# Optimization experiments

Hardware: AMD Instinct MI355X
Metric: run time of the kernel (lower is better)

Reference implementation:

```python
import jax, jax.numpy as jnp
import numpy as np

V, D, C, H = 32, 128, 2048, 8
B, M = 8, 2048
HD = D // H


def rms_norm(x, scale):
    # Whole-tensor (per-batch) RMS over dims (1,2), as in the source (quirky but faithful).
    Bx, Mx, Dx = x.shape
    fr = jnp.sqrt(jnp.sum(x * x, axis=(1, 2))) * (Mx * Dx) ** -0.5  # (B,)
    raw = x / fr[:, None, None]
    return scale[:Mx, :][None, :, :] * raw


def rope_tables(Mx):
    i = jnp.arange(D // 2, dtype=jnp.float32)
    # NOTE: faithful to source: exponent uses (i-1), not i.
    base = jnp.power(10000.0, -2.0 * (i - 1.0) / D)  # (D/2,)
    pos = jnp.arange(Mx, dtype=jnp.float32)
    ang = pos[:, None] * base[None, :]  # (M, D/2)
    return jnp.cos(ang), jnp.sin(ang)


def apply_rope(t, cos, sin):
    # Equivalent to bmm with the block-diagonal 2x2 rotation matrices:
    # out[2i]   =  t[2i]*cos + t[2i+1]*sin
    # out[2i+1] = -t[2i]*sin + t[2i+1]*cos
    te, to = t[..., 0::2], t[..., 1::2]
    oe = te * cos + to * sin
    oo = -te * sin + to * cos
    return jnp.stack([oe, oo], axis=-1).reshape(t.shape)


def mha(q, k, v, in_w, in_b, out_w, out_b):
    Bx, Mx, _ = q.shape
    qp = q @ in_w[:D].T + in_b[:D]
    kp = k @ in_w[D:2 * D].T + in_b[D:2 * D]
    vp = v @ in_w[2 * D:].T + in_b[2 * D:]
    qh = qp.reshape(Bx, Mx, H, HD).transpose(0, 2, 1, 3)
    kh = kp.reshape(Bx, Mx, H, HD).transpose(0, 2, 1, 3)
    vh = vp.reshape(Bx, Mx, H, HD).transpose(0, 2, 1, 3)
    scores = jnp.einsum('bhqd,bhkd->bhqk', qh, kh) / jnp.sqrt(jnp.float32(HD))
    causal = jnp.tril(jnp.ones((Mx, Mx), dtype=bool))
    scores = jnp.where(causal[None, None], scores, -jnp.inf)
    probs = jax.nn.softmax(scores, axis=-1)  # dropout=0.1 in train mode; eval here
    o = jnp.einsum('bhqk,bhkd->bhqd', probs, vh)
    o = o.transpose(0, 2, 1, 3).reshape(Bx, Mx, D)
    return o @ out_w.T + out_b


def setup_inputs():
    key = jax.random.key(0)
    ks = jax.random.split(key, 12)
    s = 0.02
    return {
        'idx': jax.random.randint(ks[0], (B, M), 0, V),
        'targets': jax.random.randint(ks[1], (B, M), 0, V),
        'emb': jax.random.normal(ks[2], (V, D), jnp.float32) * s,
        'rms_scale': jnp.ones((C, D), jnp.float32),
        'Wq': jax.random.normal(ks[3], (D, D), jnp.float32) * s,
        'Wk': jax.random.normal(ks[4], (D, D), jnp.float32) * s,
        'Wv': jax.random.normal(ks[5], (D, D), jnp.float32) * s,
        'in_proj_w': jax.random.normal(ks[6], (3 * D, D), jnp.float32) * s,
        'in_proj_b': jnp.zeros((3 * D,), jnp.float32),
        'out_proj_w': jax.random.normal(ks[7], (D, D), jnp.float32) * s,
        'out_proj_b': jnp.zeros((D,), jnp.float32),
        'lin_w': jax.random.normal(ks[8], (D, D), jnp.float32) * s,
        'lin_b': jnp.zeros((D,), jnp.float32),
        'out_w': jax.random.normal(ks[9], (V, D), jnp.float32) * s,
        'out_b': jnp.zeros((V,), jnp.float32),
    }


def reference(idx, targets, emb, rms_scale, Wq, Wk, Wv, in_proj_w, in_proj_b,
              out_proj_w, out_proj_b, lin_w, lin_b, out_w, out_b):
    x = emb[idx]                                  # (B, M, D)
    x = rms_norm(x, rms_scale)
    Q = x @ Wq.T
    K = x @ Wk.T
    Vv = x @ Wv.T
    cos, sin = rope_tables(x.shape[1])
    q_out = apply_rope(Q, cos, sin)
    k_out = apply_rope(K, cos, sin)
    v_out = apply_rope(Vv, cos, sin)              # source rotates V too (faithful)
    x = x + mha(q_out, k_out, v_out, in_proj_w, in_proj_b, out_proj_w, out_proj_b)
    x = rms_norm(x, rms_scale)
    x = x + jax.nn.relu(x @ lin_w.T + lin_b)
    logits = x @ out_w.T + out_b                  # (B, M, V)
    logp = jax.nn.log_softmax(logits, axis=-1)
    nll = -jnp.take_along_axis(logp, targets[..., None], axis=-1)[..., 0]
    loss = jnp.mean(nll)
    return logits, loss
```

## Files before the change

kernel.cpp:

```cpp
#include <hip/hip_runtime.h>
#include <hip/hip_bf16.h>
#include <math.h>

#define Vv   32
#define Dd   128
#define Hh   8
#define Bb   8
#define Mm   2048
#define BM   (Bb*Mm)
#define NEL  (BM*Dd)
#define XNS  140
#define QKS  396

typedef _Float16 half4_t __attribute__((ext_vector_type(4)));
typedef _Float16 half8_t __attribute__((ext_vector_type(8)));
typedef __fp16   fp16x2  __attribute__((ext_vector_type(2)));
typedef float    float4_t __attribute__((ext_vector_type(4)));
#define MFMA16 __builtin_amdgcn_mfma_f32_16x16x16f16
#define MFMA32 __builtin_amdgcn_mfma_f32_16x16x32_f16

#if __has_builtin(__builtin_amdgcn_exp2f)
__device__ __forceinline__ float fexp2(float x) { return __builtin_amdgcn_exp2f(x); }
#else
__device__ __forceinline__ float fexp2(float x) { return __expf(x * 0.6931471805599453f); }
#endif

__global__ __launch_bounds__(256) void front_kernel(const float* __restrict__ Wq,
                                                    const float* __restrict__ Wk,
                                                    const float* __restrict__ Wv,
                                                    const float* __restrict__ in_w,
                                                    const float* __restrict__ out_pw,
                                                    const float* __restrict__ lin_w,
                                                    const float* __restrict__ out_w,
                                                    _Float16* __restrict__ Wh,
                                                    float* __restrict__ cosT,
                                                    float* __restrict__ sinT,
                                                    const int* __restrict__ idx,
                                                    const float* __restrict__ emb,
                                                    float* __restrict__ partials,
                                                    float* __restrict__ lossOut) {
    __shared__ float wsum[4];
    if (blockIdx.x < 1040) {
        if (blockIdx.x == 0 && threadIdx.x == 0) lossOut[0] = 0.f;
        int gid = blockIdx.x * 256 + threadIdx.x;
        if (gid < 135168) {
            const float* src;
            int i;
            if (gid < 131072) {
                int seg = gid >> 14; i = gid & 16383;
                src = seg == 0 ? Wq : seg == 1 ? Wk : seg == 2 ? Wv :
                      seg < 6 ? in_w + (size_t)(seg - 3) * 16384 :
                      seg == 6 ? out_pw : lin_w;
            } else { src = out_w; i = gid - 131072; }
            int tile = i >> 8, within = i & 255;
            int nt = tile >> 3, kk = tile & 7;
            int r = within >> 4, cc = within & 15;
            Wh[gid] = (_Float16)src[(nt * 16 + r) * 128 + kk * 16 + cc];
        } else {
            int rid = gid - 135168;
            int i = rid & 63, m = rid >> 6;
            float ex = -2.0f * ((float)i - 1.0f) / 128.0f;
            float basef = expf(ex * 9.210340371976184f);
            float ang = (float)m * basef;
            cosT[rid] = cosf(ang);
            sinT[rid] = sinf(ang);
        }
    } else {
        int blk = blockIdx.x - 1040;
        int gid = blk * 256 + threadIdx.x;
        int token = gid >> 5, t4 = gid & 31;
        float4 x = *(const float4*)(emb + (size_t)idx[token] * 128 + t4 * 4);
        float v = x.x * x.x + x.y * x.y + x.z * x.z + x.w * x.w;
        #pragma unroll
        for (int off = 32; off; off >>= 1) v += __shfl_xor(v, off);
        int lane = threadIdx.x & 63, wave = threadIdx.x >> 6;
        if (lane == 0) wsum[wave] = v;
        __syncthreads();
        if (threadIdx.x == 0) partials[blk] = wsum[0] + wsum[1] + wsum[2] + wsum[3];
    }
}

__global__ __launch_bounds__(512, 4) void gemm_qkvproj_kernel(const int* __restrict__ idx,
                                                              const float* __restrict__ emb,
                                                              const float* __restrict__ scale,
                                                              const float* __restrict__ part1,
                                                              const _Float16* __restrict__ Whqkv,
                                                              const _Float16* __restrict__ Whin,
                                                              const float* __restrict__ in_b,
                                                              const float* __restrict__ cosT,
                                                              const float* __restrict__ sinT,
                                                              _Float16* __restrict__ xnh,
                                                              _Float16* __restrict__ Qp,
                                                              _Float16* __restrict__ Kp,
                                                              _Float16* __restrict__ Vp) {
    __shared__ _Float16 xn[32 * XNS];
    __shared__ _Float16 qkv[32 * QKS];
    __shared__ float wsum0[8];
    int tid = threadIdx.x;
    int row0 = blockIdx.x * 32;
    {
        float v = (tid < 256) ? part1[(row0 >> 11) * 256 + tid] : 0.f;
        #pragma unroll
        for (int off = 32; off; off >>= 1) v += __shfl_xor(v, off);
        if ((tid & 63) == 0) wsum0[tid >> 6] = v;
    }
    __syncthreads();
    float iv = 512.0f / sqrtf(((wsum0[0] + wsum0[1]) + (wsum0[2] + wsum0[3])) +
                              ((wsum0[4] + wsum0[5]) + (wsum0[6] + wsum0[7])));
    {
        int rw = tid >> 4, c8 = (tid & 15) * 8;
        int m = (row0 + rw) & (Mm - 1);
        const float* ep = emb + (size_t)idx[row0 + rw] * 128 + c8;
        float4 xa = *(const float4*)ep;
        float4 xb = *(const float4*)(ep + 4);
        const float* sp = scale + (size_t)m * 128 + c8;
        float4 s0 = *(const float4*)sp;
        float4 s1 = *(const float4*)(sp + 4);
        half8_t o8;
        o8[0] = (_Float16)(xa.x * iv * s0.x);
        o8[1] = (_Float16)(xa.y * iv * s0.y);
        o8[2] = (_Float16)(xa.z * iv * s0.z);
        o8[3] = (_Float16)(xa.w * iv * s0.w);
        o8[4] = (_Float16)(xb.x * iv * s1.x);
        o8[5] = (_Float16)(xb.y * iv * s1.y);
        o8[6] = (_Float16)(xb.z * iv * s1.z);
        o8[7] = (_Float16)(xb.w * iv * s1.w);
        *(half8_t*)(xn + rw * XNS + c8) = o8;
        *(half8_t*)(xnh + (size_t)(row0 + rw) * 128 + c8) = o8;
    }
    __syncthreads();
    int wave = tid >> 6, lane = tid & 63;
    int r = lane & 15, c = lane >> 4;
    int nb = wave * 48;
    int aoff = c * 8;
    int boff = r * 16 + (c & 1) * 8;
    int bsel = c >> 1;
    {
        float4_t acc[2][3];
        #pragma unroll
        for (int rt = 0; rt < 2; rt++)
            #pragma unroll
            for (int t = 0; t < 3; t++) acc[rt][t] = (float4_t){0.f, 0.f, 0.f, 0.f};
        #pragma unroll
        for (int kk = 0; kk < 4; kk++) {
            half8_t a0 = *(const half8_t*)(xn + r * XNS + kk * 32 + aoff);
            half8_t a1 = *(const half8_t*)(xn + (16 + r) * XNS + kk * 32 + aoff);
            half8_t wf[3];
            #pragma unroll
            for (int t = 0; t < 3; t++)
                wf[t] = *(const half8_t*)(Whqkv + ((wave * 3 + t) * 8 + kk * 2 + bsel) * 256 + boff);
            #pragma unroll
            for (int t = 0; t < 3; t++) {
                acc[0][t] = MFMA32(a0, wf[t], acc[0][t], 0, 0, 0);
                acc[1][t] = MFMA32(a1, wf[t], acc[1][t], 0, 0, 0);
            }
        }
        #pragma unroll
        for (int rt = 0; rt < 2; rt++) {
            #pragma unroll
            for (int t = 0; t < 3; t++) {
                int n = nb + t * 16 + r;
                int ci = (n & 127) >> 1;
                #pragma unroll
                for (int reg = 0; reg < 4; reg++) {
                    int m2 = (row0 + rt * 16 + 4 * c + reg) & (Mm - 1);
                    float v = acc[rt][t][reg];
                    float vp = __shfl_xor(v, 1);
                    float cs = cosT[m2 * 64 + ci], sn = sinT[m2 * 64 + ci];
                    v = (n & 1) ? (-vp * sn + v * cs) : (v * cs + vp * sn);
                    qkv[(rt * 16 + 4 * c + reg) * QKS + n] = (_Float16)v;
                }
            }
        }
    }
    __syncthreads();
    {
        int seg_lo = nb >> 7;
        int seg_hi = (nb + 32) >> 7;
        float4_t acc[2][3];
        #pragma unroll
        for (int rt = 0; rt < 2; rt++)
            #pragma unroll
            for (int t = 0; t < 3; t++) acc[rt][t] = (float4_t){0.f, 0.f, 0.f, 0.f};
        #pragma unroll
        for (int kk = 0; kk < 4; kk++) {
            half8_t al0 = *(const half8_t*)(qkv + r * QKS + seg_lo * 128 + kk * 32 + aoff);
            half8_t al1 = *(const half8_t*)(qkv + (16 + r) * QKS + seg_lo * 128 + kk * 32 + aoff);
            half8_t ah0 = *(const half8_t*)(qkv + r * QKS + seg_hi * 128 + kk * 32 + aoff);
            half8_t ah1 = *(const half8_t*)(qkv + (16 + r) * QKS + seg_hi * 128 + kk * 32 + aoff);
            #pragma unroll
            for (int t = 0; t < 3; t++) {
                int colg = nb + t * 16;
                int seg = colg >> 7;
                int ntl = (colg & 127) >> 4;
                half8_t wf = *(const half8_t*)(Whin + ((seg * 8 + ntl) * 8 + kk * 2 + bsel) * 256 + boff);
                bool lo = (seg == seg_lo);
                acc[0][t] = MFMA32(lo ? al0 : ah0, wf, acc[0][t], 0, 0, 0);
                acc[1][t] = MFMA32(lo ? al1 : ah1, wf, acc[1][t], 0, 0, 0);
            }
        }
        int bb = row0 >> 11;
        #pragma unroll
        for (int rt = 0; rt < 2; rt++) {
            int t16 = ((row0 + rt * 16) & 2047) >> 4;
            #pragma unroll
            for (int t = 0; t < 3; t++) {
                int colg = nb + t * 16;
                int seg = colg >> 7;
                int h = (colg & 127) >> 4;
                size_t tb = ((size_t)(bb * 8 + h) * 128 + t16) * 256;
                float bv = in_b[colg + r];
                _Float16* dst = seg == 0 ? Qp : seg == 1 ? Kp : Vp;
                #pragma unroll
                for (int reg = 0; reg < 4; reg++) {
                    float v = acc[rt][t][reg] + bv;
                    int key = 4 * c + reg;
                    if (seg < 2) dst[tb + key * 16 + r] = (_Float16)v;
                    else         dst[tb + r * 16 + key] = (_Float16)v;
                }
            }
        }
    }
}

__global__ __launch_bounds__(512, 4) void gemm_ep1_kernel(const _Float16* __restrict__ Oh,
                                                          const _Float16* __restrict__ W6,
                                                          const float* __restrict__ bias,
                                                          const _Float16* __restrict__ xnh,
                                                          _Float16* __restrict__ xresh,
                                                          float* __restrict__ partials) {
    __shared__ _Float16 At[32 * XNS];
    int tid = threadIdx.x;
    int row0 = blockIdx.x * 32;
    {
        int rw = tid >> 4, c8 = (tid & 15) * 8;
        *(half8_t*)(At + rw * XNS + c8) = *(const half8_t*)(Oh + (size_t)(row0 + rw) * 128 + c8);
    }
    __syncthreads();
    int wave = tid >> 6, lane = tid & 63;
    int r = lane & 15, c = lane >> 4;
    int aoff = c * 8;
    int boff = r * 16 + (c & 1) * 8;
    int bsel = c >> 1;
    int n0 = wave * 16;
    float4_t acc[2];
    acc[0] = (float4_t){0.f, 0.f, 0.f, 0.f};
    acc[1] = (float4_t){0.f, 0.f, 0.f, 0.f};
    #pragma unroll
    for (int kk = 0; kk < 4; kk++) {
        half8_t a0 = *(const half8_t*)(At + r * XNS + kk * 32 + aoff);
        half8_t a1 = *(const half8_t*)(At + (16 + r) * XNS + kk * 32 + aoff);
        half8_t wf = *(const half8_t*)(W6 + (wave * 8 + kk * 2 + bsel) * 256 + boff);
        acc[0] = MFMA32(a0, wf, acc[0], 0, 0, 0);
        acc[1] = MFMA32(a1, wf, acc[1], 0, 0, 0);
    }
    float lssq = 0.f;
    int n = n0 + r;
    float bv = bias[n];
    #pragma unroll
    for (int rt = 0; rt < 2; rt++) {
        #pragma unroll
        for (int reg = 0; reg < 4; reg++) {
            int row = row0 + rt * 16 + 4 * c + reg;
            float v = acc[rt][reg] + bv + (float)xnh[(size_t)row * 128 + n];
            lssq += v * v;
            xresh[(size_t)row * 128 + n] = (_Float16)v;
        }
    }
    #pragma unroll
    for (int off = 32; off; off >>= 1) lssq += __shfl_xor(lssq, off);
    __shared__ float wsum[8];
    if (lane == 0) wsum[wave] = lssq;
    __syncthreads();
    if (tid == 0) partials[blockIdx.x] = ((wsum[0] + wsum[1]) + (wsum[2] + wsum[3])) +
                                        ((wsum[4] + wsum[5]) + (wsum[6] + wsum[7]));
}

__global__ __launch_bounds__(512, 4) void gemm_ep2_logits_kernel(const _Float16* __restrict__ xresh,
                                                                 const float* __restrict__ scale,
                                                                 const float* __restrict__ part2,
                                                                 const _Float16* __restrict__ W7,
                                                                 const float* __restrict__ bias,
                                                                 const _Float16* __restrict__ Wo16,
                                                                 const float* __restrict__ bo,
                                                                 const int* __restrict__ targets,
                                                                 float* __restrict__ logits,
                                                                 float* __restrict__ lossOut) {
    __shared__ _Float16 At[32 * XNS];
    __shared__ _Float16 Ao[32 * XNS];
    __shared__ float wn[2];
    int tid = threadIdx.x;
    int row0 = blockIdx.x * 32;
    float pv = part2[(row0 >> 11) * 64 + (tid & 63)];
    #pragma unroll
    for (int off = 32; off; off >>= 1) pv += __shfl_xor(pv, off);
    float iv = 512.0f / sqrtf(pv);
    {
        int rw = tid >> 4, c8 = (tid & 15) * 8;
        int m = (row0 + rw) & (Mm - 1);
        half8_t x8 = *(const half8_t*)(xresh + (size_t)(row0 + rw) * 128 + c8);
        const float* sp = scale + (size_t)m * 128 + c8;
        float4 s0 = *(const float4*)sp;
        float4 s1 = *(const float4*)(sp + 4);
        half8_t o8;
        o8[0] = (_Float16)((float)x8[0] * iv * s0.x);
        o8[1] = (_Float16)((float)x8[1] * iv * s0.y);
        o8[2] = (_Float16)((float)x8[2] * iv * s0.z);
        o8[3] = (_Float16)((float)x8[3] * iv * s0.w);
        o8[4] = (_Float16)((float)x8[4] * iv * s1.x);
        o8[5] = (_Float16)((float)x8[5] * iv * s1.y);
        o8[6] = (_Float16)((float)x8[6] * iv * s1.z);
        o8[7] = (_Float16)((float)x8[7] * iv * s1.w);
        *(half8_t*)(At + rw * XNS + c8) = o8;
    }
    __syncthreads();
    int wave = tid >> 6, lane = tid & 63;
    int r = lane & 15, c = lane >> 4;
    int aoff = c * 8;
    int boff = r * 16 + (c & 1) * 8;
    int bsel = c >> 1;
    int n0 = wave * 16;
    float4_t acc[2];
    acc[0] = (float4_t){0.f, 0.f, 0.f, 0.f};
    acc[1] = (float4_t){0.f, 0.f, 0.f, 0.f};
    #pragma unroll
    for (int kk = 0; kk < 4; kk++) {
        half8_t a0 = *(const half8_t*)(At + r * XNS + kk * 32 + aoff);
        half8_t a1 = *(const half8_t*)(At + (16 + r) * XNS + kk * 32 + aoff);
        half8_t wf = *(const half8_t*)(W7 + (wave * 8 + kk * 2 + bsel) * 256 + boff);
        acc[0] = MFMA32(a0, wf, acc[0], 0, 0, 0);
        acc[1] = MFMA32(a1, wf, acc[1], 0, 0, 0);
    }
    int n = n0 + r;
    float bv = bias[n];
    #pragma unroll
    for (int rt = 0; rt < 2; rt++) {
        #pragma unroll
        for (int reg = 0; reg < 4; reg++) {
            int row = row0 + rt * 16 + 4 * c + reg;
            int rowl = rt * 16 + 4 * c + reg;
            float v = fmaxf(acc[rt][reg] + bv, 0.f) + (float)xresh[(size_t)row * 128 + n];
            Ao[rowl * XNS + n] = (_Float16)v;
        }
    }
    __syncthreads();
    if (wave < 2) {
        int rloc = wave * 16;
        half8_t af[4];
        #pragma unroll
        for (int kk = 0; kk < 4; kk++)
            af[kk] = *(const half8_t*)(Ao + (rloc + r) * XNS + kk * 32 + aoff);
        float4_t lacc[2];
        lacc[0] = (float4_t){0.f, 0.f, 0.f, 0.f};
        lacc[1] = (float4_t){0.f, 0.f, 0.f, 0.f};
        #pragma unroll
        for (int kk = 0; kk < 4; kk++) {
            #pragma unroll
            for (int t = 0; t < 2; t++) {
                half8_t wf = *(const half8_t*)(Wo16 + (t * 8 + kk * 2 + bsel) * 256 + boff);
                lacc[t] = MFMA32(af[kk], wf, lacc[t], 0, 0, 0);
            }
        }
        float b0 = bo[r], b1 = bo[r + 16];
        float nll_s = 0.f;
        #pragma unroll
        for (int reg = 0; reg < 4; reg++) {
            int row = row0 + rloc + 4 * c + reg;
            float l0 = lacc[0][reg] + b0;
            float l1 = lacc[1][reg] + b1;
            logits[(size_t)row * 32 + r] = l0;
            logits[(size_t)row * 32 + 16 + r] = l1;
            float mx = fmaxf(l0, l1);
            #pragma unroll
            for (int off = 8; off; off >>= 1) mx = fmaxf(mx, __shfl_xor(mx, off));
            float se = __expf(l0 - mx) + __expf(l1 - mx);
            #pragma unroll
            for (int off = 8; off; off >>= 1) se += __shfl_xor(se, off);
            int tgt = targets[row];
            float sel = (tgt & 16) ? l1 : l0;
            float tval = __shfl(sel, (lane & 48) | (tgt & 15));
            nll_s += logf(se) + mx - tval;
        }
        nll_s += __shfl_xor(nll_s, 16);
        nll_s += __shfl_xor(nll_s, 32);
        if (lane == 0) wn[wave] = nll_s;
    }
    __syncthreads();
    if (tid == 0) atomicAdd(lossOut, (wn[0] + wn[1]) * (1.0f / (float)BM));
}

__device__ __forceinline__ half4_t attn_exps(float4_t st, float& ls) {
    float p0 = fexp2(st[0]), p1 = fexp2(st[1]);
    float p2 = fexp2(st[2]), p3 = fexp2(st[3]);
    ls += (p0 + p1) + (p2 + p3);
    fp16x2 lo = __builtin_amdgcn_cvt_pkrtz(p0, p1);
    fp16x2 hi = __builtin_amdgcn_cvt_pkrtz(p2, p3);
    half4_t pf;
    pf[0] = (_Float16)lo[0]; pf[1] = (_Float16)lo[1];
    pf[2] = (_Float16)hi[0]; pf[3] = (_Float16)hi[1];
    return pf;
}
__device__ __forceinline__ half4_t attn_exps_masked(float4_t st, float& ls, int r, int c) {
    float p0 = (4 * c + 0 <= r) ? fexp2(st[0]) : 0.f;
    float p1 = (4 * c + 1 <= r) ? fexp2(st[1]) : 0.f;
    float p2 = (4 * c + 2 <= r) ? fexp2(st[2]) : 0.f;
    float p3 = (4 * c + 3 <= r) ? fexp2(st[3]) : 0.f;
    ls += (p0 + p1) + (p2 + p3);
    fp16x2 lo = __builtin_amdgcn_cvt_pkrtz(p0, p1);
    fp16x2 hi = __builtin_amdgcn_cvt_pkrtz(p2, p3);
    half4_t pf;
    pf[0] = (_Float16)lo[0]; pf[1] = (_Float16)lo[1];
    pf[2] = (_Float16)hi[0]; pf[3] = (_Float16)hi[1];
    return pf;
}

__global__ __launch_bounds__(256) void attn_kernel(const _Float16* __restrict__ Qp,
                                                   const _Float16* __restrict__ Kp,
                                                   const _Float16* __restrict__ Vp,
                                                   _Float16* __restrict__ Oh) {
    __shared__ float mrg[2][10][64];
    int wave = threadIdx.x >> 6, lane = threadIdx.x & 63;
    int pair = blockIdx.x * 2 + (wave >> 1);
    int split = wave & 1;
    int qa = pair & 63, bh = pair >> 6, qb = 127 - qa;
    int r = lane & 15, c = lane >> 4;
    int lofs = r * 16 + 4 * c;
    const _Float16* Kb = Kp + (size_t)bh * 32768 + lofs;
    const _Float16* Vb = Vp + (size_t)bh * 32768 + lofs;
    const _Float16* Qb = Qp + (size_t)bh * 32768 + lofs;
    half4_t qfa = *(const half4_t*)(Qb + qa * 256);
    half4_t qfb = *(const half4_t*)(Qb + qb * 256);
    const _Float16 qscale = (_Float16)0.36067376f;
    qfa *= qscale;
    qfb *= qscale;
    float4_t zero = {0.f, 0.f, 0.f, 0.f};
    float4_t oa = zero, ob = zero;
    float lsa = 0.f, lsb = 0.f;

    for (int kt = split; kt < qa; kt += 2) {
        half4_t k0 = *(const half4_t*)(Kb + (size_t)kt * 256);
        half4_t v0 = *(const half4_t*)(Vb + (size_t)kt * 256);
        float4_t sa = MFMA16(k0, qfa, zero, 0, 0, 0);
        float4_t sb = MFMA16(k0, qfb, zero, 0, 0, 0);
        half4_t pa = attn_exps(sa, lsa);
        half4_t pb = attn_exps(sb, lsb);
        oa = MFMA16(pa, v0, oa, 0, 0, 0);
        ob = MFMA16(pb, v0, ob, 0, 0, 0);
    }
    if ((qa & 1) == split) {
        half4_t k0 = *(const half4_t*)(Kb + (size_t)qa * 256);
        half4_t v0 = *(const half4_t*)(Vb + (size_t)qa * 256);
        float4_t sa = MFMA16(k0, qfa, zero, 0, 0, 0);
        float4_t sb = MFMA16(k0, qfb, zero, 0, 0, 0);
        half4_t pa = attn_exps_masked(sa, lsa, r, c);
        half4_t pb = attn_exps(sb, lsb);
        oa = MFMA16(pa, v0, oa, 0, 0, 0);
        ob = MFMA16(pb, v0, ob, 0, 0, 0);
    }
    {
        int s = qa + 1;
        if ((s & 1) != split) s++;
        for (int kt = s; kt < qb; kt += 2) {
            half4_t k0 = *(const half4_t*)(Kb + (size_t)kt * 256);
            half4_t v0 = *(const half4_t*)(Vb + (size_t)kt * 256);
            float4_t sb = MFMA16(k0, qfb, zero, 0, 0, 0);
            half4_t pb = attn_exps(sb, lsb);
            ob = MFMA16(pb, v0, ob, 0, 0, 0);
        }
    }
    if ((qb & 1) == split) {
        half4_t k0 = *(const half4_t*)(Kb + (size_t)qb * 256);
        half4_t v0 = *(const half4_t*)(Vb + (size_t)qb * 256);
        float4_t sb = MFMA16(k0, qfb, zero, 0, 0, 0);
        half4_t pb = attn_exps_masked(sb, lsb, r, c);
        ob = MFMA16(pb, v0, ob, 0, 0, 0);
    }
    int pib = wave >> 1;
    if (split == 1) {
        #pragma unroll
        for (int i = 0; i < 4; i++) {
            mrg[pib][i][lane] = oa[i];
            mrg[pib][4 + i][lane] = ob[i];
        }
        mrg[pib][8][lane] = lsa;
        mrg[pib][9][lane] = lsb;
    }
    __syncthreads();
    if (split == 0) {
        #pragma unroll
        for (int i = 0; i < 4; i++) {
            oa[i] += mrg[pib][i][lane];
            ob[i] += mrg[pib][4 + i][lane];
        }
        lsa += mrg[pib][8][lane];
        lsb += mrg[pib][9][lane];
        lsa += __shfl_xor(lsa, 16); lsa += __shfl_xor(lsa, 32);
        lsb += __shfl_xor(lsb, 16); lsb += __shfl_xor(lsb, 32);
        int b = bh >> 3, h = bh & 7;
        #pragma unroll
        for (int reg = 0; reg < 4; reg++) {
            float la = __shfl(lsa, 4 * c + reg);
            float lb = __shfl(lsb, 4 * c + reg);
            Oh[(size_t)(b * Mm + qa * 16 + 4 * c + reg) * 128 + h * 16 + r] = (_Float16)(oa[reg] / la);
            Oh[(size_t)(b * Mm + qb * 16 + 4 * c + reg) * 128 + h * 16 + r] = (_Float16)(ob[reg] / lb);
        }
    }
}

extern "C" void kernel_launch(void* const* d_in, const int* in_sizes, int n_in,
                              void* d_out, int out_size, void* d_ws, size_t ws_size,
                              hipStream_t stream) {
    const int*   idx       = (const int*)d_in[0];
    const int*   targets   = (const int*)d_in[1];
    const float* emb       = (const float*)d_in[2];
    const float* rms_scale = (const float*)d_in[3];
    const float* Wq        = (const float*)d_in[4];
    const float* Wk        = (const float*)d_in[5];
    const float* Wv        = (const float*)d_in[6];
    const float* in_w      = (const float*)d_in[7];
    const float* in_b      = (const float*)d_in[8];
    const float* out_pw    = (const float*)d_in[9];
    const float* out_pb    = (const float*)d_in[10];
    const float* lin_w     = (const float*)d_in[11];
    const float* lin_b     = (const float*)d_in[12];
    const float* out_w     = (const float*)d_in[13];
    const float* out_b     = (const float*)d_in[14];
    float* out = (float*)d_out;
    float* lossOut = out + (size_t)BM * Vv;

    char* base = (char*)d_ws;
    const size_t MB = 1024 * 1024;
    _Float16* xnh   = (_Float16*)(base + 4 * MB);
    _Float16* Oh    = (_Float16*)(base + 8 * MB);
    _Float16* xresh = (_Float16*)(base + 12 * MB);
    _Float16* Qp    = (_Float16*)(base + 20 * MB);
    _Float16* Kp    = (_Float16*)(base + 24 * MB);
    _Float16* Vp    = (_Float16*)(base + 28 * MB);
    float*    cosT  = (float*)(base + 32 * MB);
    float*    sinT  = cosT + Mm * 64;
    float*    part1 = sinT + Mm * 64;
    float*    part2 = part1 + 2048;
    _Float16* Wh    = (_Float16*)(part2 + 512);

    front_kernel<<<1040 + 2048, 256, 0, stream>>>(Wq, Wk, Wv, in_w, out_pw, lin_w, out_w,
                                                  Wh, cosT, sinT, idx, emb, part1, lossOut);

    gemm_qkvproj_kernel<<<BM / 32, 512, 0, stream>>>(idx, emb, rms_scale, part1,
                                                     Wh, Wh + 3 * 16384, in_b,
                                                     cosT, sinT, xnh, Qp, Kp, Vp);

    attn_kernel<<<4096 / 2, 256, 0, stream>>>(Qp, Kp, Vp, Oh);

    gemm_ep1_kernel<<<BM / 32, 512, 0, stream>>>(Oh, Wh + 6 * 16384, out_pb, xnh, xresh, part2);

    gemm_ep2_logits_kernel<<<BM / 32, 512, 0, stream>>>(xresh, rms_scale, part2,
                                                        Wh + 7 * 16384, lin_b,
                                                        Wh + 131072, out_b, targets,
                                                        out, lossOut);
}
```

Measured before the change: 150.1 us.

## Drop front kernel: in-kernel fp32 weight conversion, on-the-fly RoPE, histogram-based RMS

Removes the separate front kernel that pre-converted weights to fp16 tiles, built cos/sin tables and computed per-batch sum-of-squares partials. The GEMM kernels now load fp32 weights directly and convert to half in registers. RoPE tables are computed per block in shared memory. The first RMS norm is computed from a token-count histogram times per-vocab-row squared norms. Also drops LDS staging of A operands in the epilogue GEMMs. This saves a launch and a global round-trip, but adds redundant per-block transcendental and weight-conversion work.

```diff
diff --git a/kernel.cpp b/kernel.cpp
--- a/kernel.cpp
+++ b/kernel.cpp
@@ -8,9 +8,9 @@
 #define Bb   8
 #define Mm   2048
 #define BM   (Bb*Mm)
-#define NEL  (BM*Dd)
 #define XNS  140
 #define QKS  396
+#define RPS  65
 
 typedef _Float16 half4_t __attribute__((ext_vector_type(4)));
 typedef _Float16 half8_t __attribute__((ext_vector_type(8)));
@@ -25,95 +25,86 @@
 __device__ __forceinline__ float fexp2(float x) { return __expf(x * 0.6931471805599453f); }
 #endif
 
-__global__ __launch_bounds__(256) void front_kernel(const float* __restrict__ Wq,
-                                                    const float* __restrict__ Wk,
-                                                    const float* __restrict__ Wv,
-                                                    const float* __restrict__ in_w,
-                                                    const float* __restrict__ out_pw,
-                                                    const float* __restrict__ lin_w,
-                                                    const float* __restrict__ out_w,
-                                                    _Float16* __restrict__ Wh,
-                                                    float* __restrict__ cosT,
-                                                    float* __restrict__ sinT,
-                                                    const int* __restrict__ idx,
-                                                    const float* __restrict__ emb,
-                                                    float* __restrict__ partials,
-                                                    float* __restrict__ lossOut) {
-    __shared__ float wsum[4];
-    if (blockIdx.x < 1040) {
-        if (blockIdx.x == 0 && threadIdx.x == 0) lossOut[0] = 0.f;
-        int gid = blockIdx.x * 256 + threadIdx.x;
-        if (gid < 135168) {
-            const float* src;
-            int i;
-            if (gid < 131072) {
-                int seg = gid >> 14; i = gid & 16383;
-                src = seg == 0 ? Wq : seg == 1 ? Wk : seg == 2 ? Wv :
-                      seg < 6 ? in_w + (size_t)(seg - 3) * 16384 :
-                      seg == 6 ? out_pw : lin_w;
-            } else { src = out_w; i = gid - 131072; }
-            int tile = i >> 8, within = i & 255;
-            int nt = tile >> 3, kk = tile & 7;
-            int r = within >> 4, cc = within & 15;
-            Wh[gid] = (_Float16)src[(nt * 16 + r) * 128 + kk * 16 + cc];
-        } else {
-            int rid = gid - 135168;
-            int i = rid & 63, m = rid >> 6;
-            float ex = -2.0f * ((float)i - 1.0f) / 128.0f;
-            float basef = expf(ex * 9.210340371976184f);
-            float ang = (float)m * basef;
-            cosT[rid] = cosf(ang);
-            sinT[rid] = sinf(ang);
-        }
-    } else {
-        int blk = blockIdx.x - 1040;
-        int gid = blk * 256 + threadIdx.x;
-        int token = gid >> 5, t4 = gid & 31;
-        float4 x = *(const float4*)(emb + (size_t)idx[token] * 128 + t4 * 4);
-        float v = x.x * x.x + x.y * x.y + x.z * x.z + x.w * x.w;
-        #pragma unroll
-        for (int off = 32; off; off >>= 1) v += __shfl_xor(v, off);
-        int lane = threadIdx.x & 63, wave = threadIdx.x >> 6;
-        if (lane == 0) wsum[wave] = v;
-        __syncthreads();
-        if (threadIdx.x == 0) partials[blk] = wsum[0] + wsum[1] + wsum[2] + wsum[3];
-    }
+__device__ __forceinline__ half8_t ldwf32(const float* __restrict__ W, int nt, int kslot,
+                                          int r, int wcol) {
+    const float* p = W + (nt * 16 + r) * 128 + kslot * 16 + wcol;
+    float4 w0 = *(const float4*)p;
+    float4 w1 = *(const float4*)(p + 4);
+    half8_t h;
+    h[0] = (_Float16)w0.x; h[1] = (_Float16)w0.y; h[2] = (_Float16)w0.z; h[3] = (_Float16)w0.w;
+    h[4] = (_Float16)w1.x; h[5] = (_Float16)w1.y; h[6] = (_Float16)w1.z; h[7] = (_Float16)w1.w;
+    return h;
 }
 
 __global__ __launch_bounds__(512, 4) void gemm_qkvproj_kernel(const int* __restrict__ idx,
                                                               const float* __restrict__ emb,
                                                               const float* __restrict__ scale,
-                                                              const float* __restrict__ part1,
-                                                              const _Float16* __restrict__ Whqkv,
-                                                              const _Float16* __restrict__ Whin,
+                                                              const float* __restrict__ Wq,
+                                                              const float* __restrict__ Wk,
+                                                              const float* __restrict__ Wv,
+                                                              const float* __restrict__ in_w,
                                                               const float* __restrict__ in_b,
-                                                              const float* __restrict__ cosT,
-                                                              const float* __restrict__ sinT,
                                                               _Float16* __restrict__ xnh,
                                                               _Float16* __restrict__ Qp,
                                                               _Float16* __restrict__ Kp,
-                                                              _Float16* __restrict__ Vp) {
+                                                              _Float16* __restrict__ Vp,
+                                                              float* __restrict__ lossOut) {
     __shared__ _Float16 xn[32 * XNS];
     __shared__ _Float16 qkv[32 * QKS];
-    __shared__ float wsum0[8];
+    __shared__ float ropeC[32 * RPS];
+    __shared__ float ropeS[32 * RPS];
+    __shared__ int   hcnt[32];
+    __shared__ float hn2[32];
+    __shared__ float ssqSh;
     int tid = threadIdx.x;
     int row0 = blockIdx.x * 32;
+    int b = row0 >> 11;
+    int mbase = row0 & (Mm - 1);
+    if (blockIdx.x == 0 && tid == 0) lossOut[0] = 0.f;
+    if (tid < 32) hcnt[tid] = 0;
+    #pragma unroll
+    for (int k2 = 0; k2 < 4; k2++) {
+        int e = tid * 4 + k2;
+        int mloc = e >> 6, i = e & 63;
+        float ex = -2.0f * ((float)i - 1.0f) / 128.0f;
+        float basef = expf(ex * 9.210340371976184f);
+        float ang = (float)(mbase + mloc) * basef;
+        ropeC[mloc * RPS + i] = cosf(ang);
+        ropeS[mloc * RPS + i] = sinf(ang);
+    }
+    __syncthreads();
     {
-        float v = (tid < 256) ? part1[(row0 >> 11) * 256 + tid] : 0.f;
-        #pragma unroll
-        for (int off = 32; off; off >>= 1) v += __shfl_xor(v, off);
-        if ((tid & 63) == 0) wsum0[tid >> 6] = v;
-    }
-    __syncthreads();
-    float iv = 512.0f / sqrtf(((wsum0[0] + wsum0[1]) + (wsum0[2] + wsum0[3])) +
-                              ((wsum0[4] + wsum0[5]) + (wsum0[6] + wsum0[7])));
+        const int* ib = idx + b * Mm;
+        #pragma unroll
+        for (int k2 = 0; k2 < 4; k2++) atomicAdd(&hcnt[ib[tid * 4 + k2]], 1);
+    }
+    if (tid < 256) {
+        int v = tid >> 3, part = tid & 7;
+        const float* ep = emb + v * 128 + part * 16;
+        float s = 0.f;
+        #pragma unroll
+        for (int q = 0; q < 4; q++) {
+            float4 x = *(const float4*)(ep + q * 4);
+            s += x.x * x.x + x.y * x.y + x.z * x.z + x.w * x.w;
+        }
+        s += __shfl_xor(s, 1); s += __shfl_xor(s, 2); s += __shfl_xor(s, 4);
+        if (part == 0) hn2[v] = s;
+    }
+    __syncthreads();
+    if (tid < 64) {
+        float t = (tid < 32) ? (float)hcnt[tid] * hn2[tid] : 0.f;
+        #pragma unroll
+        for (int off = 16; off; off >>= 1) t += __shfl_xor(t, off);
+        if (tid == 0) ssqSh = t;
+    }
+    __syncthreads();
+    float iv = 512.0f / sqrtf(ssqSh);
     {
         int rw = tid >> 4, c8 = (tid & 15) * 8;
-        int m = (row0 + rw) & (Mm - 1);
         const float* ep = emb + (size_t)idx[row0 + rw] * 128 + c8;
         float4 xa = *(const float4*)ep;
         float4 xb = *(const float4*)(ep + 4);
-        const float* sp = scale + (size_t)m * 128 + c8;
+        const float* sp = scale + (size_t)(mbase + rw) * 128 + c8;
         float4 s0 = *(const float4*)sp;
         float4 s1 = *(const float4*)(sp + 4);
         half8_t o8;
@@ -133,7 +124,7 @@
     int r = lane & 15, c = lane >> 4;
     int nb = wave * 48;
     int aoff = c * 8;
-    int boff = r * 16 + (c & 1) * 8;
+    int wcol = (c & 1) * 8;
     int bsel = c >> 1;
     {
         float4_t acc[2][3];
@@ -147,8 +138,11 @@
             half8_t a1 = *(const half8_t*)(xn + (16 + r) * XNS + kk * 32 + aoff);
             half8_t wf[3];
             #pragma unroll
-            for (int t = 0; t < 3; t++)
-                wf[t] = *(const half8_t*)(Whqkv + ((wave * 3 + t) * 8 + kk * 2 + bsel) * 256 + boff);
+            for (int t = 0; t < 3; t++) {
+                int gt = wave * 3 + t;
+                const float* W = gt < 8 ? Wq : gt < 16 ? Wk : Wv;
+                wf[t] = ldwf32(W, gt & 7, kk * 2 + bsel, r, wcol);
+            }
             #pragma unroll
             for (int t = 0; t < 3; t++) {
                 acc[0][t] = MFMA32(a0, wf[t], acc[0][t], 0, 0, 0);
@@ -163,12 +157,12 @@
                 int ci = (n & 127) >> 1;
                 #pragma unroll
                 for (int reg = 0; reg < 4; reg++) {
-                    int m2 = (row0 + rt * 16 + 4 * c + reg) & (Mm - 1);
+                    int mloc = rt * 16 + 4 * c + reg;
                     float v = acc[rt][t][reg];
                     float vp = __shfl_xor(v, 1);
-                    float cs = cosT[m2 * 64 + ci], sn = sinT[m2 * 64 + ci];
+                    float cs = ropeC[mloc * RPS + ci], sn = ropeS[mloc * RPS + ci];
                     v = (n & 1) ? (-vp * sn + v * cs) : (v * cs + vp * sn);
-                    qkv[(rt * 16 + 4 * c + reg) * QKS + n] = (_Float16)v;
+                    qkv[mloc * QKS + n] = (_Float16)v;
                 }
             }
         }
@@ -193,22 +187,21 @@
                 int colg = nb + t * 16;
                 int seg = colg >> 7;
                 int ntl = (colg & 127) >> 4;
-                half8_t wf = *(const half8_t*)(Whin + ((seg * 8 + ntl) * 8 + kk * 2 + bsel) * 256 + boff);
+                half8_t wf = ldwf32(in_w + seg * 16384, ntl, kk * 2 + bsel, r, wcol);
                 bool lo = (seg == seg_lo);
                 acc[0][t] = MFMA32(lo ? al0 : ah0, wf, acc[0][t], 0, 0, 0);
                 acc[1][t] = MFMA32(lo ? al1 : ah1, wf, acc[1][t], 0, 0, 0);
             }
         }
-        int bb = row0 >> 11;
         #pragma unroll
         for (int rt = 0; rt < 2; rt++) {
-            int t16 = ((row0 + rt * 16) & 2047) >> 4;
+            int t16 = (mbase + rt * 16) >> 4;
             #pragma unroll
             for (int t = 0; t < 3; t++) {
                 int colg = nb + t * 16;
                 int seg = colg >> 7;
                 int h = (colg & 127) >> 4;
-                size_t tb = ((size_t)(bb * 8 + h) * 128 + t16) * 256;
+                size_t tb = ((size_t)(b * 8 + h) * 128 + t16) * 256;
                 float bv = in_b[colg + r];
                 _Float16* dst = seg == 0 ? Qp : seg == 1 ? Kp : Vp;
                 #pragma unroll
@@ -224,23 +217,17 @@
 }
 
 __global__ __launch_bounds__(512, 4) void gemm_ep1_kernel(const _Float16* __restrict__ Oh,
-                                                          const _Float16* __restrict__ W6,
+                                                          const float* __restrict__ out_pw,
                                                           const float* __restrict__ bias,
                                                           const _Float16* __restrict__ xnh,
                                                           _Float16* __restrict__ xresh,
                                                           float* __restrict__ partials) {
-    __shared__ _Float16 At[32 * XNS];
     int tid = threadIdx.x;
     int row0 = blockIdx.x * 32;
-    {
-        int rw = tid >> 4, c8 = (tid & 15) * 8;
-        *(half8_t*)(At + rw * XNS + c8) = *(const half8_t*)(Oh + (size_t)(row0 + rw) * 128 + c8);
-    }
-    __syncthreads();
     int wave = tid >> 6, lane = tid & 63;
     int r = lane & 15, c = lane >> 4;
     int aoff = c * 8;
-    int boff = r * 16 + (c & 1) * 8;
+    int wcol = (c & 1) * 8;
     int bsel = c >> 1;
     int n0 = wave * 16;
     float4_t acc[2];
@@ -248,9 +235,9 @@
     acc[1] = (float4_t){0.f, 0.f, 0.f, 0.f};
     #pragma unroll
     for (int kk = 0; kk < 4; kk++) {
-        half8_t a0 = *(const half8_t*)(At + r * XNS + kk * 32 + aoff);
-        half8_t a1 = *(const half8_t*)(At + (16 + r) * XNS + kk * 32 + aoff);
-        half8_t wf = *(const half8_t*)(W6 + (wave * 8 + kk * 2 + bsel) * 256 + boff);
+        half8_t a0 = *(const half8_t*)(Oh + (size_t)(row0 + r) * 128 + kk * 32 + aoff);
+        half8_t a1 = *(const half8_t*)(Oh + (size_t)(row0 + 16 + r) * 128 + kk * 32 + aoff);
+        half8_t wf = ldwf32(out_pw, wave, kk * 2 + bsel, r, wcol);
         acc[0] = MFMA32(a0, wf, acc[0], 0, 0, 0);
         acc[1] = MFMA32(a1, wf, acc[1], 0, 0, 0);
     }
@@ -279,14 +266,13 @@
 __global__ __launch_bounds__(512, 4) void gemm_ep2_logits_kernel(const _Float16* __restrict__ xresh,
                                                                  const float* __restrict__ scale,
                                                                  const float* __restrict__ part2,
-                                                                 const _Float16* __restrict__ W7,
+                                                                 const float* __restrict__ lin_w,
                                                                  const float* __restrict__ bias,
-                                                                 const _Float16* __restrict__ Wo16,
+                                                                 const float* __restrict__ out_w,
                                                                  const float* __restrict__ bo,
                                                                  const int* __restrict__ targets,
                                                                  float* __restrict__ logits,
                                                                  float* __restrict__ lossOut) {
-    __shared__ _Float16 At[32 * XNS];
     __shared__ _Float16 Ao[32 * XNS];
     __shared__ float wn[2];
     int tid = threadIdx.x;
@@ -295,41 +281,43 @@
     #pragma unroll
     for (int off = 32; off; off >>= 1) pv += __shfl_xor(pv, off);
     float iv = 512.0f / sqrtf(pv);
-    {
-        int rw = tid >> 4, c8 = (tid & 15) * 8;
-        int m = (row0 + rw) & (Mm - 1);
-        half8_t x8 = *(const half8_t*)(xresh + (size_t)(row0 + rw) * 128 + c8);
-        const float* sp = scale + (size_t)m * 128 + c8;
-        float4 s0 = *(const float4*)sp;
-        float4 s1 = *(const float4*)(sp + 4);
-        half8_t o8;
-        o8[0] = (_Float16)((float)x8[0] * iv * s0.x);
-        o8[1] = (_Float16)((float)x8[1] * iv * s0.y);
-        o8[2] = (_Float16)((float)x8[2] * iv * s0.z);
-        o8[3] = (_Float16)((float)x8[3] * iv * s0.w);
-        o8[4] = (_Float16)((float)x8[4] * iv * s1.x);
-        o8[5] = (_Float16)((float)x8[5] * iv * s1.y);
-        o8[6] = (_Float16)((float)x8[6] * iv * s1.z);
-        o8[7] = (_Float16)((float)x8[7] * iv * s1.w);
-        *(half8_t*)(At + rw * XNS + c8) = o8;
-    }
-    __syncthreads();
     int wave = tid >> 6, lane = tid & 63;
     int r = lane & 15, c = lane >> 4;
     int aoff = c * 8;
-    int boff = r * 16 + (c & 1) * 8;
+    int wcol = (c & 1) * 8;
     int bsel = c >> 1;
+    half8_t af[2][4];
+    #pragma unroll
+    for (int rt = 0; rt < 2; rt++) {
+        int row = row0 + rt * 16 + r;
+        const _Float16* xp = xresh + (size_t)row * 128;
+        const float* sp = scale + (size_t)(row & (Mm - 1)) * 128;
+        #pragma unroll
+        for (int kk = 0; kk < 4; kk++) {
+            half8_t x8 = *(const half8_t*)(xp + kk * 32 + aoff);
+            float4 s0 = *(const float4*)(sp + kk * 32 + aoff);
+            float4 s1 = *(const float4*)(sp + kk * 32 + aoff + 4);
+            half8_t o8;
+            o8[0] = (_Float16)((float)x8[0] * iv * s0.x);
+            o8[1] = (_Float16)((float)x8[1] * iv * s0.y);
+            o8[2] = (_Float16)((float)x8[2] * iv * s0.z);
+            o8[3] = (_Float16)((float)x8[3] * iv * s0.w);
+            o8[4] = (_Float16)((float)x8[4] * iv * s1.x);
+            o8[5] = (_Float16)((float)x8[5] * iv * s1.y);
+            o8[6] = (_Float16)((float)x8[6] * iv * s1.z);
+            o8[7] = (_Float16)((float)x8[7] * iv * s1.w);
+            af[rt][kk] = o8;
+        }
+    }
     int n0 = wave * 16;
     float4_t acc[2];
     acc[0] = (float4_t){0.f, 0.f, 0.f, 0.f};
     acc[1] = (float4_t){0.f, 0.f, 0.f, 0.f};
     #pragma unroll
     for (int kk = 0; kk < 4; kk++) {
-        half8_t a0 = *(const half8_t*)(At + r * XNS + kk * 32 + aoff);
-        half8_t a1 = *(const half8_t*)(At + (16 + r) * XNS + kk * 32 + aoff);
-        half8_t wf = *(const half8_t*)(W7 + (wave * 8 + kk * 2 + bsel) * 256 + boff);
-        acc[0] = MFMA32(a0, wf, acc[0], 0, 0, 0);
-        acc[1] = MFMA32(a1, wf, acc[1], 0, 0, 0);
+        half8_t wf = ldwf32(lin_w, wave, kk * 2 + bsel, r, wcol);
+        acc[0] = MFMA32(af[0][kk], wf, acc[0], 0, 0, 0);
+        acc[1] = MFMA32(af[1][kk], wf, acc[1], 0, 0, 0);
     }
     int n = n0 + r;
     float bv = bias[n];
@@ -346,10 +334,10 @@
     __syncthreads();
     if (wave < 2) {
         int rloc = wave * 16;
-        half8_t af[4];
+        half8_t lf[4];
         #pragma unroll
         for (int kk = 0; kk < 4; kk++)
-            af[kk] = *(const half8_t*)(Ao + (rloc + r) * XNS + kk * 32 + aoff);
+            lf[kk] = *(const half8_t*)(Ao + (rloc + r) * XNS + kk * 32 + aoff);
         float4_t lacc[2];
         lacc[0] = (float4_t){0.f, 0.f, 0.f, 0.f};
         lacc[1] = (float4_t){0.f, 0.f, 0.f, 0.f};
@@ -357,8 +345,8 @@
         for (int kk = 0; kk < 4; kk++) {
             #pragma unroll
             for (int t = 0; t < 2; t++) {
-                half8_t wf = *(const half8_t*)(Wo16 + (t * 8 + kk * 2 + bsel) * 256 + boff);
-                lacc[t] = MFMA32(af[kk], wf, lacc[t], 0, 0, 0);
+                half8_t wf = ldwf32(out_w, t, kk * 2 + bsel, r, wcol);
+                lacc[t] = MFMA32(lf[kk], wf, lacc[t], 0, 0, 0);
             }
         }
         float b0 = bo[r], b1 = bo[r + 16];
@@ -536,25 +524,18 @@
     _Float16* Qp    = (_Float16*)(base + 20 * MB);
     _Float16* Kp    = (_Float16*)(base + 24 * MB);
     _Float16* Vp    = (_Float16*)(base + 28 * MB);
-    float*    cosT  = (float*)(base + 32 * MB);
-    float*    sinT  = cosT + Mm * 64;
-    float*    part1 = sinT + Mm * 64;
-    float*    part2 = part1 + 2048;
-    _Float16* Wh    = (_Float16*)(part2 + 512);
-
-    front_kernel<<<1040 + 2048, 256, 0, stream>>>(Wq, Wk, Wv, in_w, out_pw, lin_w, out_w,
-                                                  Wh, cosT, sinT, idx, emb, part1, lossOut);
-
-    gemm_qkvproj_kernel<<<BM / 32, 512, 0, stream>>>(idx, emb, rms_scale, part1,
-                                                     Wh, Wh + 3 * 16384, in_b,
-                                                     cosT, sinT, xnh, Qp, Kp, Vp);
+    float*    part2 = (float*)(base + 32 * MB);
+
+    gemm_qkvproj_kernel<<<BM / 32, 512, 0, stream>>>(idx, emb, rms_scale,
+                                                     Wq, Wk, Wv, in_w, in_b,
+                                                     xnh, Qp, Kp, Vp, lossOut);
 
     attn_kernel<<<4096 / 2, 256, 0, stream>>>(Qp, Kp, Vp, Oh);
 
-    gemm_ep1_kernel<<<BM / 32, 512, 0, stream>>>(Oh, Wh + 6 * 16384, out_pb, xnh, xresh, part2);
+    gemm_ep1_kernel<<<BM / 32, 512, 0, stream>>>(Oh, out_pw, out_pb, xnh, xresh, part2);
 
     gemm_ep2_logits_kernel<<<BM / 32, 512, 0, stream>>>(xresh, rms_scale, part2,
-                                                        Wh + 7 * 16384, lin_b,
-                                                        Wh + 131072, out_b, targets,
+                                                        lin_w, lin_b,
+                                                        out_w, out_b, targets,
                                                         out, lossOut);
 }
```

New measurement: 183.3 us. +22.1%, slower.

## Compute per-batch RMS sum via token histogram over the 32-entry embedding table

Applied to the files above, without the earlier changes.

The first RMS norm's sum of squares over a batch now comes from a per-batch histogram of token ids, weighted by each embedding row's squared norm. This replaces the 2048 blocks that gathered every token's embedding with 8 blocks that each count 2048 ids using shared-memory atomics. It also removes the per-block reduction of 256 partials in the QKV projection kernel, which now reads one value per batch. The cost is shared-memory atomic contention across only 32 bins and a different floating-point summation order.

```diff
diff --git a/kernel.cpp b/kernel.cpp
--- a/kernel.cpp
+++ b/kernel.cpp
@@ -8,7 +8,6 @@
 #define Bb   8
 #define Mm   2048
 #define BM   (Bb*Mm)
-#define NEL  (BM*Dd)
 #define XNS  140
 #define QKS  396
 
@@ -39,7 +38,6 @@
                                                     const float* __restrict__ emb,
                                                     float* __restrict__ partials,
                                                     float* __restrict__ lossOut) {
-    __shared__ float wsum[4];
     if (blockIdx.x < 1040) {
         if (blockIdx.x == 0 && threadIdx.x == 0) lossOut[0] = 0.f;
         int gid = blockIdx.x * 256 + threadIdx.x;
@@ -66,17 +64,36 @@
             sinT[rid] = sinf(ang);
         }
     } else {
-        int blk = blockIdx.x - 1040;
-        int gid = blk * 256 + threadIdx.x;
-        int token = gid >> 5, t4 = gid & 31;
-        float4 x = *(const float4*)(emb + (size_t)idx[token] * 128 + t4 * 4);
-        float v = x.x * x.x + x.y * x.y + x.z * x.z + x.w * x.w;
-        #pragma unroll
-        for (int off = 32; off; off >>= 1) v += __shfl_xor(v, off);
-        int lane = threadIdx.x & 63, wave = threadIdx.x >> 6;
-        if (lane == 0) wsum[wave] = v;
+        int b = blockIdx.x - 1040;
+        __shared__ int   hc[4][32];
+        __shared__ float n2[32];
+        int tid = threadIdx.x;
+        int wave = tid >> 6;
+        if (tid < 128) ((int*)hc)[tid] = 0;
         __syncthreads();
-        if (threadIdx.x == 0) partials[blk] = wsum[0] + wsum[1] + wsum[2] + wsum[3];
+        const int* ib = idx + b * Mm;
+        #pragma unroll
+        for (int k = 0; k < 8; k++) atomicAdd(&hc[wave][ib[tid * 8 + k]], 1);
+        {
+            int v = tid >> 3, part = tid & 7;
+            const float* ep = emb + v * 128 + part * 16;
+            float s = 0.f;
+            #pragma unroll
+            for (int q = 0; q < 4; q++) {
+                float4 x = *(const float4*)(ep + q * 4);
+                s += x.x * x.x + x.y * x.y + x.z * x.z + x.w * x.w;
+            }
+            s += __shfl_xor(s, 1); s += __shfl_xor(s, 2); s += __shfl_xor(s, 4);
+            if (part == 0) n2[v] = s;
+        }
+        __syncthreads();
+        if (tid < 32) {
+            int cnt = ((hc[0][tid] + hc[1][tid]) + (hc[2][tid] + hc[3][tid]));
+            float t = (float)cnt * n2[tid];
+            #pragma unroll
+            for (int off = 16; off; off >>= 1) t += __shfl_xor(t, off);
+            if (tid == 0) partials[b] = t;
+        }
     }
 }
 
@@ -95,18 +112,9 @@
                                                               _Float16* __restrict__ Vp) {
     __shared__ _Float16 xn[32 * XNS];
     __shared__ _Float16 qkv[32 * QKS];
-    __shared__ float wsum0[8];
     int tid = threadIdx.x;
     int row0 = blockIdx.x * 32;
-    {
-        float v = (tid < 256) ? part1[(row0 >> 11) * 256 + tid] : 0.f;
-        #pragma unroll
-        for (int off = 32; off; off >>= 1) v += __shfl_xor(v, off);
-        if ((tid & 63) == 0) wsum0[tid >> 6] = v;
-    }
-    __syncthreads();
-    float iv = 512.0f / sqrtf(((wsum0[0] + wsum0[1]) + (wsum0[2] + wsum0[3])) +
-                              ((wsum0[4] + wsum0[5]) + (wsum0[6] + wsum0[7])));
+    float iv = 512.0f / sqrtf(part1[row0 >> 11]);
     {
         int rw = tid >> 4, c8 = (tid & 15) * 8;
         int m = (row0 + rw) & (Mm - 1);
@@ -346,10 +354,10 @@
     __syncthreads();
     if (wave < 2) {
         int rloc = wave * 16;
-        half8_t af[4];
+        half8_t lf[4];
         #pragma unroll
         for (int kk = 0; kk < 4; kk++)
-            af[kk] = *(const half8_t*)(Ao + (rloc + r) * XNS + kk * 32 + aoff);
+            lf[kk] = *(const half8_t*)(Ao + (rloc + r) * XNS + kk * 32 + aoff);
         float4_t lacc[2];
         lacc[0] = (float4_t){0.f, 0.f, 0.f, 0.f};
         lacc[1] = (float4_t){0.f, 0.f, 0.f, 0.f};
@@ -358,7 +366,7 @@
             #pragma unroll
             for (int t = 0; t < 2; t++) {
                 half8_t wf = *(const half8_t*)(Wo16 + (t * 8 + kk * 2 + bsel) * 256 + boff);
-                lacc[t] = MFMA32(af[kk], wf, lacc[t], 0, 0, 0);
+                lacc[t] = MFMA32(lf[kk], wf, lacc[t], 0, 0, 0);
             }
         }
         float b0 = bo[r], b1 = bo[r + 16];
@@ -542,8 +550,8 @@
     float*    part2 = part1 + 2048;
     _Float16* Wh    = (_Float16*)(part2 + 512);
 
-    front_kernel<<<1040 + 2048, 256, 0, stream>>>(Wq, Wk, Wv, in_w, out_pw, lin_w, out_w,
-                                                  Wh, cosT, sinT, idx, emb, part1, lossOut);
+    front_kernel<<<1040 + 8, 256, 0, stream>>>(Wq, Wk, Wv, in_w, out_pw, lin_w, out_w,
+                                               Wh, cosT, sinT, idx, emb, part1, lossOut);
 
     gemm_qkvproj_kernel<<<BM / 32, 512, 0, stream>>>(idx, emb, rms_scale, part1,
                                                      Wh, Wh + 3 * 16384, in_b,
```

New measurement: 151.6 us. Within noise of the previous version (+1.0%).
